# Kernel optimization log

Hardware: AMD Instinct MI355X
Metric: run time of the kernel (lower is better)

The kernel has to match this reference:

```python
import jax, jax.numpy as jnp
import numpy as np

B, S, F_IN, H, NH, NL, HOR = 8, 128, 128, 256, 8, 4, 24


def _ln(x, g, b, eps=1e-5):
    m = jnp.mean(x, axis=-1, keepdims=True)
    v = jnp.var(x, axis=-1, keepdims=True)
    return (x - m) / jnp.sqrt(v + eps) * g + b


def setup_inputs() -> dict:
    key = jax.random.key(0)
    cnt = [0]
    def nrm(shape, scale=0.02):
        cnt[0] += 1
        return jax.random.normal(jax.random.fold_in(key, cnt[0]), shape, jnp.float32) * scale
    d = {}
    d['x'] = jax.random.normal(jax.random.fold_in(key, 999), (B, S, F_IN), jnp.float32)
    # flattened GRN (input F_IN -> hidden H -> output F_IN)
    d['fg_w1'] = nrm((F_IN, H)); d['fg_b1'] = nrm((H,))
    d['fg_w2'] = nrm((H, H));    d['fg_b2'] = nrm((H,))
    d['fg_wo'] = nrm((H, F_IN)); d['fg_bo'] = nrm((F_IN,))
    d['fg_wg'] = nrm((H, F_IN)); d['fg_bg'] = nrm((F_IN,))
    d['fg_sw'] = nrm((F_IN, F_IN)); d['fg_sb'] = nrm((F_IN,))
    d['fg_lng'] = jnp.ones((F_IN,)); d['fg_lnb'] = jnp.zeros((F_IN,))
    # stacked per-variable GRNs (input 1 -> hidden H -> output H), F_IN of them
    d['sv_w1'] = nrm((F_IN, H)); d['sv_b1'] = nrm((F_IN, H))
    d['sv_w2'] = nrm((F_IN, H, H)); d['sv_b2'] = nrm((F_IN, H))
    d['sv_wo'] = nrm((F_IN, H, H)); d['sv_bo'] = nrm((F_IN, H))
    d['sv_wg'] = nrm((F_IN, H, H)); d['sv_bg'] = nrm((F_IN, H))
    d['sv_sw'] = nrm((F_IN, H)); d['sv_sb'] = nrm((F_IN, H))
    d['sv_lng'] = jnp.ones((F_IN, H)); d['sv_lnb'] = jnp.zeros((F_IN, H))
    d['pos_enc'] = nrm((1000, H), 1.0)
    # 2-layer LSTM (torch gate order i,f,g,o)
    for l in (0, 1):
        d[f'l{l}_wih'] = nrm((4 * H, H)); d[f'l{l}_whh'] = nrm((4 * H, H))
        d[f'l{l}_bih'] = nrm((4 * H,));   d[f'l{l}_bhh'] = nrm((4 * H,))
    # NL attention layers, stacked
    d['att_wq'] = nrm((NL, H, H)); d['att_wk'] = nrm((NL, H, H))
    d['att_wv'] = nrm((NL, H, H)); d['att_wo'] = nrm((NL, H, H))
    d['att_bo'] = nrm((NL, H))
    d['att_lng'] = jnp.ones((NL, H)); d['att_lnb'] = jnp.zeros((NL, H))
    # output head and quantile heads
    d['out_w1'] = nrm((H, H // 2)); d['out_b1'] = nrm((H // 2,))
    d['out_w2'] = nrm((H // 2, HOR)); d['out_b2'] = nrm((HOR,))
    d['qw'] = nrm((3, H, HOR)); d['qb'] = nrm((3, HOR))
    return d


def _forward(x, fg_w1, fg_b1, fg_w2, fg_b2, fg_wo, fg_bo, fg_wg, fg_bg, fg_sw, fg_sb,
             fg_lng, fg_lnb, sv_w1, sv_b1, sv_w2, sv_b2, sv_wo, sv_bo, sv_wg, sv_bg,
             sv_sw, sv_sb, sv_lng, sv_lnb, pos_enc, l0_wih, l0_whh, l0_bih, l0_bhh,
             l1_wih, l1_whh, l1_bih, l1_bhh, att_wq, att_wk, att_wv, att_wo, att_bo,
             att_lng, att_lnb, out_w1, out_b1, out_w2, out_b2, qw, qb):
    b, s, f = x.shape
    xf = x.reshape(b * s, f)                      # [N,F]
    # ---- flattened GRN -> variable selection weights ----
    skip = xf @ fg_sw + fg_sb
    h = jax.nn.elu(xf @ fg_w1 + fg_b1)
    h = jax.nn.elu(h @ fg_w2 + fg_b2)
    sw = _ln(jax.nn.sigmoid(h @ fg_wg + fg_bg) * (h @ fg_wo + fg_bo) + skip, fg_lng, fg_lnb)
    sw = jax.nn.softmax(sw, axis=-1)              # [N,F]
    # ---- all per-variable GRNs, batched over the feature axis ----
    h1 = jax.nn.elu(xf[:, :, None] * sv_w1[None] + sv_b1[None])                 # [N,F,H]
    h2 = jax.nn.elu(jnp.einsum('nfh,fhk->nfk', h1, sv_w2) + sv_b2)              # [N,F,H]
    vo = jnp.einsum('nfh,fhk->nfk', h2, sv_wo) + sv_bo
    vg = jax.nn.sigmoid(jnp.einsum('nfh,fhk->nfk', h2, sv_wg) + sv_bg)
    vskip = xf[:, :, None] * sv_sw[None] + sv_sb[None]
    v = _ln(vg * vo + vskip, sv_lng, sv_lnb)                                    # [N,F,H]
    sel = jnp.einsum('nfh,nf->nh', v, sw)                                       # [N,H]
    feats = sel.reshape(b, s, -1) + pos_enc[:s][None]                           # [B,S,H]
    # ---- 2-layer LSTM ----
    def lstm(xseq, wih, whh, bih, bhh):
        hh = whh.shape[1]
        bias = bih + bhh
        def step(carry, xt):
            hp, cp = carry
            g = xt @ wih.T + hp @ whh.T + bias
            i, fg, gg, o = jnp.split(g, 4, axis=-1)
            c = jax.nn.sigmoid(fg) * cp + jax.nn.sigmoid(i) * jnp.tanh(gg)
            hn = jax.nn.sigmoid(o) * jnp.tanh(c)
            return (hn, c), hn
        init = (jnp.zeros((xseq.shape[0], hh), xseq.dtype),
                jnp.zeros((xseq.shape[0], hh), xseq.dtype))
        _, ys = jax.lax.scan(step, init, jnp.swapaxes(xseq, 0, 1))
        return jnp.swapaxes(ys, 0, 1)
    a = lstm(feats, l0_wih, l0_whh, l0_bih, l0_bhh)
    a = lstm(a, l1_wih, l1_whh, l1_bih, l1_bhh)
    # ---- NL self-attention layers ----
    dk = a.shape[-1] // NH
    scale = 1.0 / np.sqrt(dk)
    for l in range(att_wq.shape[0]):
        resid = a
        Q = (a @ att_wq[l]).reshape(b, s, NH, dk)
        K = (a @ att_wk[l]).reshape(b, s, NH, dk)
        V = (a @ att_wv[l]).reshape(b, s, NH, dk)
        scores = jnp.einsum('bqhd,bkhd->bhqk', Q, K) * scale
        w = jax.nn.softmax(scores, axis=-1)
        ctx = jnp.einsum('bhqk,bkhd->bqhd', w, V).reshape(b, s, -1)
        a = _ln(ctx @ att_wo[l] + att_bo[l] + resid, att_lng[l], att_lnb[l])
    gctx = jnp.mean(a, axis=1)                                                  # [B,H]
    pf = jax.nn.relu(gctx @ out_w1 + out_b1) @ out_w2 + out_b2                  # [B,HOR]
    q10 = gctx @ qw[0] + qb[0]
    q50 = gctx @ qw[1] + qb[1]
    q90 = gctx @ qw[2] + qb[2]
    return pf, q10, q50, q90, sw.reshape(b, s, -1), a


def reference(x, fg_w1, fg_b1, fg_w2, fg_b2, fg_wo, fg_bo, fg_wg, fg_bg, fg_sw, fg_sb,
              fg_lng, fg_lnb, sv_w1, sv_b1, sv_w2, sv_b2, sv_wo, sv_bo, sv_wg, sv_bg,
              sv_sw, sv_sb, sv_lng, sv_lnb, pos_enc, l0_wih, l0_whh, l0_bih, l0_bhh,
              l1_wih, l1_whh, l1_bih, l1_bhh, att_wq, att_wk, att_wv, att_wo, att_bo,
              att_lng, att_lnb, out_w1, out_b1, out_w2, out_b2, qw, qb):
    return _forward(x, fg_w1, fg_b1, fg_w2, fg_b2, fg_wo, fg_bo, fg_wg, fg_bg, fg_sw,
                    fg_sb, fg_lng, fg_lnb, sv_w1, sv_b1, sv_w2, sv_b2, sv_wo, sv_bo,
                    sv_wg, sv_bg, sv_sw, sv_sb, sv_lng, sv_lnb, pos_enc, l0_wih, l0_whh,
                    l0_bih, l0_bhh, l1_wih, l1_whh, l1_bih, l1_bhh, att_wq, att_wk,
                    att_wv, att_wo, att_bo, att_lng, att_lnb, out_w1, out_b1, out_w2,
                    out_b2, qw, qb)
```

## Files before the change

### kernel.cpp

```cpp
#include <hip/hip_runtime.h>
#include <cstdint>
#include <cstddef>

typedef __bf16 bf16;
typedef __attribute__((ext_vector_type(4))) __bf16 bf16x4;
typedef __attribute__((ext_vector_type(8))) __bf16 bf16x8;
typedef __attribute__((ext_vector_type(4))) float floatx4;

#define MFMA16(a,b,c) __builtin_amdgcn_mfma_f32_16x16x32_bf16(a,b,c,0,0,0)

__device__ __forceinline__ float sigmf_(float x){ return 1.f/(1.f+expf(-x)); }
__device__ __forceinline__ float eluf_(float x){ return x>0.f ? x : (expf(x)-1.f); }

template<int EPI>
__global__ void __launch_bounds__(256, 2)
gemm_bf16(const float* __restrict__ A, int lda,
          const bf16* __restrict__ BT, int ldb,
          float* __restrict__ C, int ldc,
          const float* __restrict__ b1, const float* __restrict__ b2r,
          int K)
{
  __shared__ char sm[16384 + 8192];
  const int tid = threadIdx.x;
  const int bm = blockIdx.y * 128, bn = blockIdx.x * 64;
  const int l = tid & 63, w = tid >> 6;
  const int wm = (w >> 1) * 64, wn = (w & 1) * 32;
  floatx4 acc[4][2];
  #pragma unroll
  for (int i = 0; i < 4; ++i)
    #pragma unroll
    for (int j = 0; j < 2; ++j)
      #pragma unroll
      for (int r = 0; r < 4; ++r) acc[i][j][r] = 0.f;

  for (int k0 = 0; k0 < K; k0 += 64) {
    {
      int r0 = tid >> 4, kq = (tid & 15) * 4;
      #pragma unroll
      for (int p = 0; p < 8; ++p) {
        int m = r0 + p * 16;
        float4 v = *(const float4*)(A + (size_t)(bm + m) * lda + k0 + kq);
        bf16x4 hv; hv[0]=(bf16)v.x; hv[1]=(bf16)v.y; hv[2]=(bf16)v.z; hv[3]=(bf16)v.w;
        unsigned off = ((unsigned)(m * 128 + kq * 2)) ^ ((unsigned)(m & 7) << 4);
        *(bf16x4*)(sm + off) = hv;
      }
      int n = tid >> 2, c = (tid & 3) * 16;
      const bf16* src = BT + (size_t)(bn + n) * ldb + k0 + c;
      bf16x8 v0 = *(const bf16x8*)(src);
      bf16x8 v1 = *(const bf16x8*)(src + 8);
      unsigned o0 = 16384u + (((unsigned)(n * 128 + c * 2))      ^ ((unsigned)(n & 7) << 4));
      unsigned o1 = 16384u + (((unsigned)(n * 128 + c * 2 + 16)) ^ ((unsigned)(n & 7) << 4));
      *(bf16x8*)(sm + o0) = v0;
      *(bf16x8*)(sm + o1) = v1;
    }
    __syncthreads();
    const int row = l & 15, kb = (l >> 4) * 8;
    #pragma unroll
    for (int kk = 0; kk < 64; kk += 32) {
      bf16x8 a[4], b[2];
      #pragma unroll
      for (int i = 0; i < 4; ++i) {
        int m = wm + i * 16 + row;
        unsigned off = ((unsigned)(m * 128 + (kk + kb) * 2)) ^ ((unsigned)(m & 7) << 4);
        a[i] = *(const bf16x8*)(sm + off);
      }
      #pragma unroll
      for (int j = 0; j < 2; ++j) {
        int n = wn + j * 16 + row;
        unsigned off = 16384u + (((unsigned)(n * 128 + (kk + kb) * 2)) ^ ((unsigned)(n & 7) << 4));
        b[j] = *(const bf16x8*)(sm + off);
      }
      #pragma unroll
      for (int i = 0; i < 4; ++i)
        #pragma unroll
        for (int j = 0; j < 2; ++j)
          acc[i][j] = MFMA16(a[i], b[j], acc[i][j]);
    }
    __syncthreads();
  }
  #pragma unroll
  for (int i = 0; i < 4; ++i)
    #pragma unroll
    for (int j = 0; j < 2; ++j)
      #pragma unroll
      for (int r = 0; r < 4; ++r) {
        int grow = bm + wm + i * 16 + ((l >> 4) << 2) + r;
        int gcol = bn + wn + j * 16 + (l & 15);
        float v = acc[i][j][r];
        if (EPI == 1) v += b1[gcol];
        else if (EPI == 2) { v += b1[gcol]; v = eluf_(v); }
        else if (EPI == 3) { v += (gcol < 128) ? b1[gcol] : b2r[gcol - 128]; }
        else if (EPI == 4) { v += b1[gcol] + b2r[(size_t)grow * ldc + gcol]; }
        C[(size_t)grow * ldc + gcol] = v;
      }
}

__device__ __forceinline__ void tile_tr64(const float* __restrict__ src, int srcld,
                                          bf16* __restrict__ dst, int dstld,
                                          float (*ld)[72])
{
  const int tid = threadIdx.x;
  const int r = tid >> 2, q = tid & 3;
  #pragma unroll
  for (int i = 0; i < 4; ++i) {
    int col = q * 16 + i * 4;
    *(float4*)&ld[r][col] = *(const float4*)(src + (size_t)r * srcld + col);
  }
  __syncthreads();
  bf16x8 o0, o1;
  #pragma unroll
  for (int i = 0; i < 8; ++i) o0[i] = (bf16)ld[q * 16 + i][r];
  #pragma unroll
  for (int i = 0; i < 8; ++i) o1[i] = (bf16)ld[q * 16 + 8 + i][r];
  *(bf16x8*)(dst + (size_t)r * dstld + q * 16) = o0;
  *(bf16x8*)(dst + (size_t)r * dstld + q * 16 + 8) = o1;
}

__global__ void __launch_bounds__(256)
transpose_sv(const float* __restrict__ w2, const float* __restrict__ wo,
             const float* __restrict__ wg, bf16* __restrict__ svT)
{
  __shared__ float ld[64][72];
  int mat = blockIdx.y >> 7;
  int f = blockIdx.y & 127;
  const float* src = (mat == 0 ? w2 : (mat == 1 ? wo : wg)) + (size_t)f * 65536;
  bf16* dst = svT + (size_t)blockIdx.y * 65536;
  int tc = blockIdx.x & 3, tr = blockIdx.x >> 2;
  tile_tr64(src + (size_t)(tr * 64) * 256 + tc * 64, 256,
            dst + (size_t)(tc * 64) * 256 + tr * 64, 256, ld);
}

struct TJob { const float* src; bf16* dst; int R; int C; };
struct TJobs { TJob j[22]; };

__global__ void __launch_bounds__(256)
transpose_misc(TJobs jobs)
{
  __shared__ float ld[64][72];
  TJob J = jobs.j[blockIdx.y];
  int ntc = J.C >> 6;
  int tiles = (J.R >> 6) * ntc;
  if ((int)blockIdx.x >= tiles) return;
  int tc = blockIdx.x % ntc, tr = blockIdx.x / ntc;
  tile_tr64(J.src + (size_t)(tr * 64) * J.C + tc * 64, J.C,
            J.dst + (size_t)(tc * 64) * J.R + tr * 64, J.R, ld);
}

__global__ void __launch_bounds__(256)
cvt4_kernel(const float* __restrict__ s0, const float* __restrict__ s1,
            const float* __restrict__ s2, const float* __restrict__ s3,
            bf16* __restrict__ dst)
{
  size_t i = ((size_t)blockIdx.x * 256 + threadIdx.x) * 4;
  int mat = (int)(i >> 18);
  const float* s = (mat == 0) ? s0 : (mat == 1) ? s1 : (mat == 2) ? s2 : s3;
  float4 v = *(const float4*)(s + (i & 262143));
  bf16x4 o; o[0]=(bf16)v.x; o[1]=(bf16)v.y; o[2]=(bf16)v.z; o[3]=(bf16)v.w;
  *(bf16x4*)(dst + i) = o;
}

__global__ void __launch_bounds__(256, 4)
grnflat_sw_kernel(const float* __restrict__ go, const float* __restrict__ skip,
                  const float* __restrict__ lng, const float* __restrict__ lnb,
                  float* __restrict__ sw_out)
{
  const int tid = threadIdx.x;
  const int m = blockIdx.x * 4 + (tid >> 6);
  const int l = tid & 63, c = l * 2;
  float g0 = go[(size_t)m * 256 + c],       g1 = go[(size_t)m * 256 + c + 1];
  float o0 = go[(size_t)m * 256 + 128 + c], o1 = go[(size_t)m * 256 + 128 + c + 1];
  float sk0 = skip[(size_t)m * 128 + c],    sk1 = skip[(size_t)m * 128 + c + 1];
  float p0 = sigmf_(g0) * o0 + sk0;
  float p1 = sigmf_(g1) * o1 + sk1;
  float s = p0 + p1, s2 = p0 * p0 + p1 * p1;
  #pragma unroll
  for (int k = 1; k < 64; k <<= 1) { s += __shfl_xor(s, k, 64); s2 += __shfl_xor(s2, k, 64); }
  float mean = s * (1.f / 128.f);
  float var = s2 * (1.f / 128.f) - mean * mean;
  float rs = rsqrtf(var + 1e-5f);
  float t0 = (p0 - mean) * rs * lng[c] + lnb[c];
  float t1 = (p1 - mean) * rs * lng[c + 1] + lnb[c + 1];
  float mx = fmaxf(t0, t1);
  #pragma unroll
  for (int k = 1; k < 64; k <<= 1) mx = fmaxf(mx, __shfl_xor(mx, k, 64));
  float e0 = expf(t0 - mx), e1 = expf(t1 - mx);
  float se = e0 + e1;
  #pragma unroll
  for (int k = 1; k < 64; k <<= 1) se += __shfl_xor(se, k, 64);
  float inv = 1.f / se;
  float2 wv; wv.x = e0 * inv; wv.y = e1 * inv;
  *(float2*)(sw_out + (size_t)m * 128 + c) = wv;
}

__global__ void __launch_bounds__(512, 2)
pervar_kernel(const bf16* __restrict__ xT, const bf16* __restrict__ svT,
              const float* __restrict__ w1g, const float* __restrict__ b1g,
              const float* __restrict__ b2g, const float* __restrict__ bog,
              const float* __restrict__ bgg, const float* __restrict__ swg,
              const float* __restrict__ sbg, const float* __restrict__ lngg,
              const float* __restrict__ lnbg,
              bf16* __restrict__ vbuf, int f0)
{
  __shared__ char sm[65536];
  const int tid = threadIdx.x;
  const int fl = blockIdx.y, f = f0 + fl, tile = blockIdx.x;
  const int l = tid & 63, w = tid >> 6;
  const int wm = (w >> 2) * 32, wn = (w & 3) * 64;
  const int row = l & 15, kb = (l >> 4) * 8;
  const size_t fb = (size_t)f * 256;

  {
    int m = tid >> 3, ks8 = (tid & 7) * 32;
    float x = (float)xT[(size_t)f * 1024 + tile * 64 + m];
    #pragma unroll
    for (int i = 0; i < 4; ++i) {
      int k = ks8 + i * 8;
      float4 w0v = *(const float4*)(w1g + fb + k);
      float4 w1v = *(const float4*)(w1g + fb + k + 4);
      float4 b0v = *(const float4*)(b1g + fb + k);
      float4 b1v = *(const float4*)(b1g + fb + k + 4);
      bf16x8 hv;
      hv[0] = (bf16)eluf_(x * w0v.x + b0v.x);
      hv[1] = (bf16)eluf_(x * w0v.y + b0v.y);
      hv[2] = (bf16)eluf_(x * w0v.z + b0v.z);
      hv[3] = (bf16)eluf_(x * w0v.w + b0v.w);
      hv[4] = (bf16)eluf_(x * w1v.x + b1v.x);
      hv[5] = (bf16)eluf_(x * w1v.y + b1v.y);
      hv[6] = (bf16)eluf_(x * w1v.z + b1v.z);
      hv[7] = (bf16)eluf_(x * w1v.w + b1v.w);
      unsigned off = ((unsigned)(m * 512 + k * 2)) ^ ((unsigned)(m & 7) << 4);
      *(bf16x8*)(sm + off) = hv;
    }
  }

  auto stageB = [&](const bf16* BT, int ks) {
    int n = tid >> 1, c = (tid & 1) * 32;
    const bf16* src = BT + (size_t)n * 256 + ks * 64 + c;
    #pragma unroll
    for (int qq = 0; qq < 4; ++qq) {
      unsigned ro = (((unsigned)(n * 128 + (c + qq * 8) * 2)) ^ ((unsigned)(n & 7) << 4));
      *(bf16x8*)(sm + 32768 + ro) = *(const bf16x8*)(src + qq * 8);
    }
  };

  floatx4 acc1[2][4];
  #pragma unroll
  for (int i = 0; i < 2; ++i)
    #pragma unroll
    for (int j = 0; j < 4; ++j)
      #pragma unroll
      for (int r = 0; r < 4; ++r) acc1[i][j][r] = 0.f;
  const bf16* w2T = svT + (size_t)f * 65536;
  for (int ks = 0; ks < 4; ++ks) {
    __syncthreads();
    stageB(w2T, ks);
    __syncthreads();
    #pragma unroll
    for (int kk = 0; kk < 64; kk += 32) {
      int kloc = kk + kb;
      bf16x8 a[2], b[4];
      #pragma unroll
      for (int i = 0; i < 2; ++i) {
        int m = wm + i * 16 + row;
        unsigned off = ((unsigned)(m * 512 + (ks * 64 + kloc) * 2)) ^ ((unsigned)(m & 7) << 4);
        a[i] = *(const bf16x8*)(sm + off);
      }
      #pragma unroll
      for (int j = 0; j < 4; ++j) {
        int n = wn + j * 16 + row;
        unsigned off = 32768u + (((unsigned)(n * 128 + kloc * 2)) ^ ((unsigned)(n & 7) << 4));
        b[j] = *(const bf16x8*)(sm + off);
      }
      #pragma unroll
      for (int i = 0; i < 2; ++i)
        #pragma unroll
        for (int j = 0; j < 4; ++j)
          acc1[i][j] = MFMA16(a[i], b[j], acc1[i][j]);
    }
  }
  __syncthreads();
  #pragma unroll
  for (int i = 0; i < 2; ++i)
    #pragma unroll
    for (int j = 0; j < 4; ++j)
      #pragma unroll
      for (int r = 0; r < 4; ++r) {
        int m = wm + i * 16 + ((l >> 4) << 2) + r;
        int col = wn + j * 16 + (l & 15);
        float v = eluf_(acc1[i][j][r] + b2g[fb + col]);
        unsigned off = ((unsigned)(m * 512 + col * 2)) ^ ((unsigned)(m & 7) << 4);
        *(bf16*)(sm + off) = (bf16)v;
      }
  __syncthreads();

  floatx4 accO[2][4], accG[2][4];
  #pragma unroll
  for (int i = 0; i < 2; ++i)
    #pragma unroll
    for (int j = 0; j < 4; ++j)
      #pragma unroll
      for (int r = 0; r < 4; ++r) { accO[i][j][r] = 0.f; accG[i][j][r] = 0.f; }
  const bf16* woT = svT + ((size_t)128 + f) * 65536;
  const bf16* wgT = svT + ((size_t)256 + f) * 65536;
  for (int ks = 0; ks < 4; ++ks) {
    __syncthreads();
    stageB(woT, ks);
    __syncthreads();
    #pragma unroll
    for (int kk = 0; kk < 64; kk += 32) {
      int kloc = kk + kb;
      bf16x8 a[2], b[4];
      #pragma unroll
      for (int i = 0; i < 2; ++i) {
        int m = wm + i * 16 + row;
        unsigned off = ((unsigned)(m * 512 + (ks * 64 + kloc) * 2)) ^ ((unsigned)(m & 7) << 4);
        a[i] = *(const bf16x8*)(sm + off);
      }
      #pragma unroll
      for (int j = 0; j < 4; ++j) {
        int n = wn + j * 16 + row;
        unsigned off = 32768u + (((unsigned)(n * 128 + kloc * 2)) ^ ((unsigned)(n & 7) << 4));
        b[j] = *(const bf16x8*)(sm + off);
      }
      #pragma unroll
      for (int i = 0; i < 2; ++i)
        #pragma unroll
        for (int j = 0; j < 4; ++j)
          accO[i][j] = MFMA16(a[i], b[j], accO[i][j]);
    }
  }
  for (int ks = 0; ks < 4; ++ks) {
    __syncthreads();
    stageB(wgT, ks);
    __syncthreads();
    #pragma unroll
    for (int kk = 0; kk < 64; kk += 32) {
      int kloc = kk + kb;
      bf16x8 a[2], b[4];
      #pragma unroll
      for (int i = 0; i < 2; ++i) {
        int m = wm + i * 16 + row;
        unsigned off = ((unsigned)(m * 512 + (ks * 64 + kloc) * 2)) ^ ((unsigned)(m & 7) << 4);
        a[i] = *(const bf16x8*)(sm + off);
      }
      #pragma unroll
      for (int j = 0; j < 4; ++j) {
        int n = wn + j * 16 + row;
        unsigned off = 32768u + (((unsigned)(n * 128 + kloc * 2)) ^ ((unsigned)(n & 7) << 4));
        b[j] = *(const bf16x8*)(sm + off);
      }
      #pragma unroll
      for (int i = 0; i < 2; ++i)
        #pragma unroll
        for (int j = 0; j < 4; ++j)
          accG[i][j] = MFMA16(a[i], b[j], accG[i][j]);
    }
  }
  __syncthreads();
  {
    float xm[2][4];
    #pragma unroll
    for (int i = 0; i < 2; ++i)
      #pragma unroll
      for (int r = 0; r < 4; ++r) {
        int m = wm + i * 16 + ((l >> 4) << 2) + r;
        xm[i][r] = (float)xT[(size_t)f * 1024 + tile * 64 + m];
      }
    #pragma unroll
    for (int i = 0; i < 2; ++i)
      #pragma unroll
      for (int j = 0; j < 4; ++j)
        #pragma unroll
        for (int r = 0; r < 4; ++r) {
          int m = wm + i * 16 + ((l >> 4) << 2) + r;
          int col = wn + j * 16 + (l & 15);
          float vg = sigmf_(accG[i][j][r] + bgg[fb + col]);
          float vo = accO[i][j][r] + bog[fb + col];
          float pre = vg * vo + xm[i][r] * swg[fb + col] + sbg[fb + col];
          unsigned off = ((unsigned)(m * 512 + col * 2)) ^ ((unsigned)(m & 7) << 4);
          *(bf16*)(sm + off) = (bf16)pre;
        }
  }
  __syncthreads();
  {
    int m = tid >> 3, q = tid & 7;
    float vals[32];
    float s = 0.f, s2 = 0.f;
    #pragma unroll
    for (int i = 0; i < 4; ++i) {
      unsigned off = ((unsigned)(m * 512 + (q * 32 + i * 8) * 2)) ^ ((unsigned)(m & 7) << 4);
      bf16x8 hv = *(const bf16x8*)(sm + off);
      #pragma unroll
      for (int j = 0; j < 8; ++j) {
        float x = (float)hv[j];
        vals[i * 8 + j] = x; s += x; s2 += x * x;
      }
    }
    s += __shfl_xor(s, 1, 64);  s += __shfl_xor(s, 2, 64);  s += __shfl_xor(s, 4, 64);
    s2 += __shfl_xor(s2, 1, 64); s2 += __shfl_xor(s2, 2, 64); s2 += __shfl_xor(s2, 4, 64);
    float mean = s * (1.f / 256.f);
    float var = s2 * (1.f / 256.f) - mean * mean;
    float rs = rsqrtf(var + 1e-5f);
    bf16* dst = vbuf + ((size_t)fl * 1024 + tile * 64 + m) * 256 + q * 32;
    #pragma unroll
    for (int i = 0; i < 4; ++i) {
      int c = q * 32 + i * 8;
      float4 g0 = *(const float4*)(lngg + fb + c);
      float4 g1 = *(const float4*)(lngg + fb + c + 4);
      float4 bb0 = *(const float4*)(lnbg + fb + c);
      float4 bb1 = *(const float4*)(lnbg + fb + c + 4);
      bf16x8 ov;
      ov[0] = (bf16)((vals[i * 8 + 0] - mean) * rs * g0.x + bb0.x);
      ov[1] = (bf16)((vals[i * 8 + 1] - mean) * rs * g0.y + bb0.y);
      ov[2] = (bf16)((vals[i * 8 + 2] - mean) * rs * g0.z + bb0.z);
      ov[3] = (bf16)((vals[i * 8 + 3] - mean) * rs * g0.w + bb0.w);
      ov[4] = (bf16)((vals[i * 8 + 4] - mean) * rs * g1.x + bb1.x);
      ov[5] = (bf16)((vals[i * 8 + 5] - mean) * rs * g1.y + bb1.y);
      ov[6] = (bf16)((vals[i * 8 + 6] - mean) * rs * g1.z + bb1.z);
      ov[7] = (bf16)((vals[i * 8 + 7] - mean) * rs * g1.w + bb1.w);
      *(bf16x8*)(dst + i * 8) = ov;
    }
  }
}

__global__ void __launch_bounds__(256, 4)
selreduce_kernel(const bf16* __restrict__ vbuf, const float* __restrict__ sw,
                 const float* __restrict__ pos, float* __restrict__ feats,
                 int f0, int FC, int flags)
{
  const int tid = threadIdx.x;
  const int m = blockIdx.x * 4 + (tid >> 6);
  const int hh = (tid & 63) * 4;
  float a0, a1, a2, a3;
  if (flags & 1) { a0 = a1 = a2 = a3 = 0.f; }
  else {
    float4 v = *(const float4*)(feats + (size_t)m * 256 + hh);
    a0 = v.x; a1 = v.y; a2 = v.z; a3 = v.w;
  }
  for (int fi = 0; fi < FC; ++fi) {
    float wgt = sw[(size_t)m * 128 + f0 + fi];
    bf16x4 v = *(const bf16x4*)(vbuf + ((size_t)fi * 1024 + m) * 256 + hh);
    a0 += wgt * (float)v[0]; a1 += wgt * (float)v[1];
    a2 += wgt * (float)v[2]; a3 += wgt * (float)v[3];
  }
  if (flags & 2) {
    float4 p = *(const float4*)(pos + (size_t)(m & 127) * 256 + hh);
    a0 += p.x; a1 += p.y; a2 += p.z; a3 += p.w;
  }
  float4 o; o.x = a0; o.y = a1; o.z = a2; o.w = a3;
  *(float4*)(feats + (size_t)m * 256 + hh) = o;
}

__global__ void __launch_bounds__(256, 1)
lstm_mfma(const bf16* __restrict__ wl, const float* __restrict__ xpre0,
          const float* __restrict__ b0a, const float* __restrict__ b0b,
          const float* __restrict__ b1a, const float* __restrict__ b1b,
          bf16* __restrict__ h0seq, bf16* __restrict__ h1seq,
          float* __restrict__ aseq, unsigned* __restrict__ ctr)
{
  __shared__ float gbuf[4][16][8];
  const int tid = threadIdx.x;
  const int l = tid & 63, w = tid >> 6;
  const int layer = blockIdx.x >> 4, U = (blockIdx.x & 15) * 16;
  const int row = w * 256 + U + (l & 15);
  const int ko = (l >> 4) * 8;
  const bf16* whh = wl + (size_t)(layer ? 3 : 1) * 262144 + (size_t)row * 256;
  const bf16* wih1 = wl + (size_t)2 * 262144 + (size_t)row * 256;
  bf16x8 bw[8], bx[8];
  #pragma unroll
  for (int kt = 0; kt < 8; ++kt) bw[kt] = *(const bf16x8*)(whh + kt * 32 + ko);
  if (layer) {
    #pragma unroll
    for (int kt = 0; kt < 8; ++kt) bx[kt] = *(const bf16x8*)(wih1 + kt * 32 + ko);
  }
  const float bsum = layer ? (b1a[row] + b1b[row]) : (b0a[row] + b0b[row]);
  bf16* hs = layer ? h1seq : h0seq;
  unsigned* c0 = ctr;
  unsigned* c1 = ctr + 128;
  unsigned* cs = layer ? c1 : c0;
  float cstate = 0.f;
  const int au = tid >> 3, ab = tid & 7;

  for (int t = 0; t < 128; ++t) {
    float xp[4] = {0.f, 0.f, 0.f, 0.f};
    if (!layer && (l >> 4) < 2) {
      #pragma unroll
      for (int r = 0; r < 4; ++r) {
        int bb = (l >> 4) * 4 + r;
        xp[r] = xpre0[((size_t)((bb << 7) | t)) * 1024 + row];
      }
    }
    if (tid == 0) {
      if (layer == 0) {
        if (t > 0)
          while (__hip_atomic_load(c0 + t - 1, __ATOMIC_ACQUIRE, __HIP_MEMORY_SCOPE_AGENT) < 16u)
            __builtin_amdgcn_s_sleep(2);
      } else {
        while (__hip_atomic_load(c0 + t, __ATOMIC_ACQUIRE, __HIP_MEMORY_SCOPE_AGENT) < 16u)
          __builtin_amdgcn_s_sleep(2);
        if (t > 0)
          while (__hip_atomic_load(c1 + t - 1, __ATOMIC_ACQUIRE, __HIP_MEMORY_SCOPE_AGENT) < 16u)
            __builtin_amdgcn_s_sleep(2);
      }
    }
    __syncthreads();
    floatx4 acc; acc[0] = acc[1] = acc[2] = acc[3] = 0.f;
    if (t > 0) {
      const bf16* hp = hs + (size_t)(t - 1) * 4096 + (size_t)(l & 15) * 256 + ko;
      #pragma unroll
      for (int kt = 0; kt < 8; ++kt)
        acc = MFMA16(*(const bf16x8*)(hp + kt * 32), bw[kt], acc);
    }
    if (layer) {
      const bf16* hp = h0seq + (size_t)t * 4096 + (size_t)(l & 15) * 256 + ko;
      #pragma unroll
      for (int kt = 0; kt < 8; ++kt)
        acc = MFMA16(*(const bf16x8*)(hp + kt * 32), bx[kt], acc);
    }
    if ((l >> 4) < 2) {
      #pragma unroll
      for (int r = 0; r < 4; ++r) {
        int bb = (l >> 4) * 4 + r;
        gbuf[w][l & 15][bb] = acc[r] + bsum + xp[r];
      }
    }
    __syncthreads();
    if (tid < 128) {
      float gi = gbuf[0][au][ab], gf = gbuf[1][au][ab];
      float gg = gbuf[2][au][ab], go = gbuf[3][au][ab];
      cstate = sigmf_(gf) * cstate + sigmf_(gi) * tanhf(gg);
      float h = sigmf_(go) * tanhf(cstate);
      hs[(size_t)t * 4096 + (size_t)ab * 256 + U + au] = (bf16)h;
      if (layer) aseq[((size_t)((ab << 7) | t)) * 256 + U + au] = h;
    }
    __syncthreads();
    if (tid == 0) {
      __threadfence();
      __hip_atomic_fetch_add(cs + t, 1u, __ATOMIC_RELEASE, __HIP_MEMORY_SCOPE_AGENT);
    }
  }
}

__global__ void __launch_bounds__(256, 2)
attn_kernel(const float* __restrict__ qkv, float* __restrict__ ctxo)
{
  __shared__ float Kb[128][40];
  __shared__ float Vb[128][40];
  const int tid = threadIdx.x;
  const int b = blockIdx.x >> 3, h = blockIdx.x & 7;
  const int s = tid >> 1, half = tid & 1;
  {
    const float* kr = qkv + ((size_t)(b * 128 + s)) * 768 + 256 + h * 32 + half * 16;
    #pragma unroll
    for (int i = 0; i < 4; ++i) {
      *(float4*)&Kb[s][half * 16 + i * 4] = *(const float4*)(kr + i * 4);
      *(float4*)&Vb[s][half * 16 + i * 4] = *(const float4*)(kr + 256 + i * 4);
    }
  }
  float q[32];
  {
    const float* qr = qkv + ((size_t)(b * 128 + s)) * 768 + h * 32;
    #pragma unroll
    for (int i = 0; i < 8; ++i) {
      float4 v = *(const float4*)(qr + i * 4);
      q[i * 4 + 0] = v.x; q[i * 4 + 1] = v.y; q[i * 4 + 2] = v.z; q[i * 4 + 3] = v.w;
    }
  }
  __syncthreads();
  const float scale = 0.17677669529663687f;
  float se = 0.f;
  float ca[32];
  #pragma unroll
  for (int i = 0; i < 32; ++i) ca[i] = 0.f;
  for (int c0 = 0; c0 < 64; ++c0) {
    int c = half * 64 + c0;
    float d = 0.f;
    #pragma unroll
    for (int i = 0; i < 32; ++i) d += q[i] * Kb[c][i];
    float e = expf(d * scale);
    se += e;
    #pragma unroll
    for (int i = 0; i < 32; ++i) ca[i] += e * Vb[c][i];
  }
  se += __shfl_xor(se, 1, 64);
  #pragma unroll
  for (int i = 0; i < 32; ++i) ca[i] += __shfl_xor(ca[i], 1, 64);
  if (half == 0) {
    float inv = 1.f / se;
    float* outp = ctxo + ((size_t)(b * 128 + s)) * 256 + h * 32;
    #pragma unroll
    for (int i = 0; i < 32; i += 4) {
      float4 v; v.x = ca[i] * inv; v.y = ca[i + 1] * inv; v.z = ca[i + 2] * inv; v.w = ca[i + 3] * inv;
      *(float4*)(outp + i) = v;
    }
  }
}

__global__ void __launch_bounds__(256, 4)
ln_kernel(const float* __restrict__ in, const float* __restrict__ g,
          const float* __restrict__ bta, float* __restrict__ out,
          float* __restrict__ mirror)
{
  const int tid = threadIdx.x;
  const int m = blockIdx.x * 4 + (tid >> 6);
  const int l = tid & 63;
  float4 v = *(const float4*)(in + (size_t)m * 256 + l * 4);
  float s = v.x + v.y + v.z + v.w;
  float s2 = v.x * v.x + v.y * v.y + v.z * v.z + v.w * v.w;
  #pragma unroll
  for (int k = 1; k < 64; k <<= 1) { s += __shfl_xor(s, k, 64); s2 += __shfl_xor(s2, k, 64); }
  float mean = s * (1.f / 256.f);
  float var = s2 * (1.f / 256.f) - mean * mean;
  float rs = rsqrtf(var + 1e-5f);
  float4 gg = *(const float4*)(g + l * 4);
  float4 bb = *(const float4*)(bta + l * 4);
  float4 o;
  o.x = (v.x - mean) * rs * gg.x + bb.x;
  o.y = (v.y - mean) * rs * gg.y + bb.y;
  o.z = (v.z - mean) * rs * gg.z + bb.z;
  o.w = (v.w - mean) * rs * gg.w + bb.w;
  *(float4*)(out + (size_t)m * 256 + l * 4) = o;
  if (mirror) *(float4*)(mirror + (size_t)m * 256 + l * 4) = o;
}

__global__ void __launch_bounds__(256)
gctx_kernel(const float* __restrict__ a, float* __restrict__ g)
{
  int b = blockIdx.x, hh = threadIdx.x;
  float s = 0.f;
  for (int ss = 0; ss < 128; ++ss) s += a[((size_t)b * 128 + ss) * 256 + hh];
  g[b * 256 + hh] = s * (1.f / 128.f);
}

__global__ void __launch_bounds__(256, 1)
head_kernel(const float* __restrict__ g, const float* __restrict__ w1,
            const float* __restrict__ b1, const float* __restrict__ w2,
            const float* __restrict__ b2, const float* __restrict__ qw,
            const float* __restrict__ qb, float* __restrict__ dout)
{
  __shared__ float hid[8][128];
  const int tid = threadIdx.x;
  for (int o = tid; o < 1024; o += 256) {
    int b = o >> 7, j = o & 127;
    float s = b1[j];
    for (int k = 0; k < 256; ++k) s += g[b * 256 + k] * w1[(size_t)k * 128 + j];
    hid[b][j] = s > 0.f ? s : 0.f;
  }
  __syncthreads();
  if (tid < 192) {
    int b = tid / 24, j = tid - b * 24;
    float s = b2[j];
    for (int k = 0; k < 128; ++k) s += hid[b][k] * w2[(size_t)k * 24 + j];
    dout[b * 24 + j] = s;
  }
  for (int o = tid; o < 576; o += 256) {
    int qi = o / 192, rr = o - qi * 192, b = rr / 24, j = rr - b * 24;
    float s = qb[qi * 24 + j];
    for (int k = 0; k < 256; ++k) s += g[b * 256 + k] * qw[((size_t)qi * 256 + k) * 24 + j];
    dout[192 + o] = s;
  }
}

extern "C" void kernel_launch(void* const* d_in, const int* in_sizes, int n_in,
                              void* d_out, int out_size, void* d_ws, size_t ws_size,
                              hipStream_t stream)
{
  (void)in_sizes; (void)n_in; (void)out_size;
  auto F = [&](int i) { return (const float*)d_in[i]; };
  char* ws = (char*)d_ws;
  size_t o = 0;
  auto alloc = [&](size_t b) { size_t r = o; o = (o + b + 255) & ~(size_t)255; return r; };

  size_t svT_o  = alloc((size_t)3 * 128 * 65536 * 2);
  size_t wl_o   = alloc((size_t)4 * 262144 * 2);
  size_t qkvT_o = alloc((size_t)4 * 196608 * 2);
  size_t woT_o  = alloc((size_t)4 * 65536 * 2);
  size_t w1T_o  = alloc(256 * 128 * 2);
  size_t w2T_o  = alloc(256 * 256 * 2);
  size_t goT_o  = alloc(256 * 256 * 2);
  size_t swT_o  = alloc(128 * 128 * 2);
  size_t xT_o   = alloc(128 * 1024 * 2);
  size_t h_o    = alloc((size_t)1024 * 256 * 4);
  size_t h2_o   = alloc((size_t)1024 * 256 * 4);
  size_t go_o   = alloc((size_t)1024 * 256 * 4);
  size_t skip_o = alloc((size_t)1024 * 128 * 4);
  size_t feat_o = alloc((size_t)1024 * 256 * 4);
  size_t xpre_o = alloc((size_t)1024 * 1024 * 4);
  size_t qkv_o  = alloc((size_t)1024 * 768 * 4);
  size_t ctx_o  = alloc((size_t)1024 * 256 * 4);
  size_t pre_o  = alloc((size_t)1024 * 256 * 4);
  size_t aA_o   = alloc((size_t)1024 * 256 * 4);
  size_t aB_o   = alloc((size_t)1024 * 256 * 4);
  size_t gctx_o = alloc(8 * 256 * 4);
  size_t z_o    = alloc((size_t)2 * 1048576 + 1024);
  size_t aseq_o = alloc((size_t)1024 * 256 * 4);
  int FC = 128;
  while (FC > 4 && o + (size_t)FC * 1024 * 256 * 2 > ws_size) FC >>= 1;
  size_t vb_o = alloc((size_t)FC * 1024 * 256 * 2);
  if (o > ws_size) return;

  bf16* svTp  = (bf16*)(ws + svT_o);
  bf16* wlp   = (bf16*)(ws + wl_o);
  bf16* qkvTp = (bf16*)(ws + qkvT_o);
  bf16* woTp  = (bf16*)(ws + woT_o);
  bf16* w1Tp  = (bf16*)(ws + w1T_o);
  bf16* w2Tp  = (bf16*)(ws + w2T_o);
  bf16* goTp  = (bf16*)(ws + goT_o);
  bf16* swTp  = (bf16*)(ws + swT_o);
  bf16* xTp   = (bf16*)(ws + xT_o);
  float* hp    = (float*)(ws + h_o);
  float* h2p   = (float*)(ws + h2_o);
  float* gop   = (float*)(ws + go_o);
  float* skipp = (float*)(ws + skip_o);
  float* featp = (float*)(ws + feat_o);
  float* xprep = (float*)(ws + xpre_o);
  float* qkvp  = (float*)(ws + qkv_o);
  float* ctxp  = (float*)(ws + ctx_o);
  float* prep  = (float*)(ws + pre_o);
  float* aAp   = (float*)(ws + aA_o);
  float* aBp   = (float*)(ws + aB_o);
  float* gctxp = (float*)(ws + gctx_o);
  bf16* h0p    = (bf16*)(ws + z_o);
  bf16* h1p    = (bf16*)(ws + z_o + 1048576);
  unsigned* ctrp = (unsigned*)(ws + z_o + 2097152);
  float* aseqp = (float*)(ws + aseq_o);
  bf16* vbp    = (bf16*)(ws + vb_o);

  float* outp  = (float*)d_out;
  float* sw_do = outp + 768;
  float* a_do  = outp + 131840;

  hipMemsetAsync(ws + z_o, 0, 2097152 + 1024, stream);

  transpose_sv<<<dim3(16, 384), 256, 0, stream>>>(F(15), F(17), F(19), svTp);
  {
    TJobs tj; int nj = 0;
    auto addj = [&](const float* s, bf16* d, int R, int C) { tj.j[nj].src = s; tj.j[nj].dst = d; tj.j[nj].R = R; tj.j[nj].C = C; ++nj; };
    for (int l = 0; l < 4; ++l) {
      addj(F(34) + (size_t)l * 65536, qkvTp + (size_t)l * 196608, 256, 256);
      addj(F(35) + (size_t)l * 65536, qkvTp + (size_t)l * 196608 + 65536, 256, 256);
      addj(F(36) + (size_t)l * 65536, qkvTp + (size_t)l * 196608 + 131072, 256, 256);
      addj(F(37) + (size_t)l * 65536, woTp + (size_t)l * 65536, 256, 256);
    }
    addj(F(1), w1Tp, 128, 256);
    addj(F(3), w2Tp, 256, 256);
    addj(F(7), goTp, 256, 128);
    addj(F(5), goTp + 128 * 256, 256, 128);
    addj(F(9), swTp, 128, 128);
    addj(F(0), xTp, 1024, 128);
    transpose_misc<<<dim3(32, 22), 256, 0, stream>>>(tj);
  }
  cvt4_kernel<<<1024, 256, 0, stream>>>(F(26), F(27), F(30), F(31), wlp);

  auto gemm = [&](int epi, const float* A, int lda, const bf16* BT, int ldb,
                  float* C, int ldc, int M, int N, int K,
                  const float* b1, const float* b2r) {
    dim3 g(N / 64, M / 128);
    switch (epi) {
      case 0: gemm_bf16<0><<<g, 256, 0, stream>>>(A, lda, BT, ldb, C, ldc, b1, b2r, K); break;
      case 1: gemm_bf16<1><<<g, 256, 0, stream>>>(A, lda, BT, ldb, C, ldc, b1, b2r, K); break;
      case 2: gemm_bf16<2><<<g, 256, 0, stream>>>(A, lda, BT, ldb, C, ldc, b1, b2r, K); break;
      case 3: gemm_bf16<3><<<g, 256, 0, stream>>>(A, lda, BT, ldb, C, ldc, b1, b2r, K); break;
      case 4: gemm_bf16<4><<<g, 256, 0, stream>>>(A, lda, BT, ldb, C, ldc, b1, b2r, K); break;
    }
  };

  gemm(2, F(0), 128, w1Tp, 128, hp, 256, 1024, 256, 128, F(2), nullptr);
  gemm(2, hp, 256, w2Tp, 256, h2p, 256, 1024, 256, 256, F(4), nullptr);
  gemm(3, h2p, 256, goTp, 256, gop, 256, 1024, 256, 256, F(8), F(6));
  gemm(1, F(0), 128, swTp, 128, skipp, 128, 1024, 128, 128, F(10), nullptr);
  grnflat_sw_kernel<<<256, 256, 0, stream>>>(gop, skipp, F(11), F(12), sw_do);

  int chunks = 128 / FC;
  for (int c = 0; c < chunks; ++c) {
    pervar_kernel<<<dim3(16, FC), 512, 0, stream>>>(
        xTp, svTp, F(13), F(14), F(16), F(18), F(20), F(21), F(22), F(23), F(24),
        vbp, c * FC);
    selreduce_kernel<<<256, 256, 0, stream>>>(
        vbp, sw_do, F(25), featp, c * FC, FC,
        (c == 0 ? 1 : 0) | (c == chunks - 1 ? 2 : 0));
  }

  gemm(0, featp, 256, wlp, 256, xprep, 1024, 1024, 1024, 256, nullptr, nullptr);
  lstm_mfma<<<32, 256, 0, stream>>>(wlp, xprep, F(28), F(29), F(32), F(33),
                                    h0p, h1p, aseqp, ctrp);

  const float* ain = aseqp;
  float* louts[4] = {aAp, aBp, aAp, aBp};
  for (int l = 0; l < 4; ++l) {
    gemm(0, ain, 256, qkvTp + (size_t)l * 196608, 256, qkvp, 768, 1024, 768, 256, nullptr, nullptr);
    attn_kernel<<<64, 256, 0, stream>>>(qkvp, ctxp);
    gemm(4, ctxp, 256, woTp + (size_t)l * 65536, 256, prep, 256, 1024, 256, 256,
         F(38) + (size_t)l * 256, ain);
    ln_kernel<<<256, 256, 0, stream>>>(prep, F(39) + (size_t)l * 256, F(40) + (size_t)l * 256,
                                       louts[l], l == 3 ? a_do : (float*)nullptr);
    ain = louts[l];
  }

  gctx_kernel<<<8, 256, 0, stream>>>(aBp, gctxp);
  head_kernel<<<1, 256, 0, stream>>>(gctxp, F(41), F(42), F(43), F(44), F(45), F(46), outp);
}
```

Before: 1.112 ms.

## Fuse QKV projection into attention and output projection with LayerNorm

Each attention block now computes its own Q/K/V slice with MFMA, reading the layer input directly, so the separate QKV GEMM and its global buffer are gone. The output projection, bias, residual add and LayerNorm are merged into one kernel where each block owns 128 full rows. This cuts four launches down to two per layer and removes intermediate global round trips. The trade-off is that every (batch, head) block re-reads its full input rows and QKV weights are loaded from global without LDS staging. The proj_ln kernel runs on only 8 blocks, which leaves most of the GPU idle.

```diff
diff --git a/kernel.cpp b/kernel.cpp
--- a/kernel.cpp
+++ b/kernel.cpp
@@ -541,32 +541,77 @@
   }
 }
 
-__global__ void __launch_bounds__(256, 2)
-attn_kernel(const float* __restrict__ qkv, float* __restrict__ ctxo)
-{
-  __shared__ float Kb[128][40];
-  __shared__ float Vb[128][40];
+__global__ void __launch_bounds__(256, 1)
+attn_qkv(const float* __restrict__ a, const bf16* __restrict__ qkvT,
+         float* __restrict__ ctxo)
+{
+  extern __shared__ char sm[];
+  float* Qb = (float*)(sm + 65536);
+  float* Kb = (float*)(sm + 86016);
+  float* Vb = (float*)(sm + 106496);
   const int tid = threadIdx.x;
   const int b = blockIdx.x >> 3, h = blockIdx.x & 7;
+  const int l = tid & 63, w = tid >> 6;
+  {
+    int m = tid >> 1, ch = (tid & 1) * 128;
+    const float* src = a + (size_t)(b * 128 + m) * 256 + ch;
+    #pragma unroll
+    for (int cc = 0; cc < 16; ++cc) {
+      float4 v0 = *(const float4*)(src + cc * 8);
+      float4 v1 = *(const float4*)(src + cc * 8 + 4);
+      bf16x8 hv;
+      hv[0]=(bf16)v0.x; hv[1]=(bf16)v0.y; hv[2]=(bf16)v0.z; hv[3]=(bf16)v0.w;
+      hv[4]=(bf16)v1.x; hv[5]=(bf16)v1.y; hv[6]=(bf16)v1.z; hv[7]=(bf16)v1.w;
+      int k = ch + cc * 8;
+      unsigned off = ((unsigned)(m * 512 + k * 2)) ^ ((unsigned)(m & 7) << 4);
+      *(bf16x8*)(sm + off) = hv;
+    }
+  }
+  __syncthreads();
+  const int row = l & 15, kb = (l >> 4) * 8;
+  floatx4 acc[2][6];
+  #pragma unroll
+  for (int i = 0; i < 2; ++i)
+    #pragma unroll
+    for (int j = 0; j < 6; ++j)
+      #pragma unroll
+      for (int r = 0; r < 4; ++r) acc[i][j][r] = 0.f;
+  for (int k0 = 0; k0 < 256; k0 += 32) {
+    int kloc = k0 + kb;
+    bf16x8 af[2];
+    #pragma unroll
+    for (int i = 0; i < 2; ++i) {
+      int m = 32 * w + 16 * i + row;
+      unsigned off = ((unsigned)(m * 512 + kloc * 2)) ^ ((unsigned)(m & 7) << 4);
+      af[i] = *(const bf16x8*)(sm + off);
+    }
+    #pragma unroll
+    for (int j = 0; j < 6; ++j) {
+      int nn = h * 32 + (j & 1) * 16 + row;
+      const bf16* bp = qkvT + (size_t)(j >> 1) * 65536 + (size_t)nn * 256 + kloc;
+      bf16x8 bf_ = *(const bf16x8*)bp;
+      #pragma unroll
+      for (int i = 0; i < 2; ++i)
+        acc[i][j] = MFMA16(af[i], bf_, acc[i][j]);
+    }
+  }
+  #pragma unroll
+  for (int i = 0; i < 2; ++i)
+    #pragma unroll
+    for (int j = 0; j < 6; ++j) {
+      float* dst = (j >> 1) == 0 ? Qb : ((j >> 1) == 1 ? Kb : Vb);
+      #pragma unroll
+      for (int r = 0; r < 4; ++r) {
+        int m = 32 * w + 16 * i + ((l >> 4) << 2) + r;
+        int nn = (j & 1) * 16 + (l & 15);
+        dst[m * 40 + nn] = acc[i][j][r];
+      }
+    }
+  __syncthreads();
   const int s = tid >> 1, half = tid & 1;
-  {
-    const float* kr = qkv + ((size_t)(b * 128 + s)) * 768 + 256 + h * 32 + half * 16;
-    #pragma unroll
-    for (int i = 0; i < 4; ++i) {
-      *(float4*)&Kb[s][half * 16 + i * 4] = *(const float4*)(kr + i * 4);
-      *(float4*)&Vb[s][half * 16 + i * 4] = *(const float4*)(kr + 256 + i * 4);
-    }
-  }
   float q[32];
-  {
-    const float* qr = qkv + ((size_t)(b * 128 + s)) * 768 + h * 32;
-    #pragma unroll
-    for (int i = 0; i < 8; ++i) {
-      float4 v = *(const float4*)(qr + i * 4);
-      q[i * 4 + 0] = v.x; q[i * 4 + 1] = v.y; q[i * 4 + 2] = v.z; q[i * 4 + 3] = v.w;
-    }
-  }
-  __syncthreads();
+  #pragma unroll
+  for (int i = 0; i < 32; ++i) q[i] = Qb[s * 40 + i];
   const float scale = 0.17677669529663687f;
   float se = 0.f;
   float ca[32];
@@ -576,11 +621,11 @@
     int c = half * 64 + c0;
     float d = 0.f;
     #pragma unroll
-    for (int i = 0; i < 32; ++i) d += q[i] * Kb[c][i];
+    for (int i = 0; i < 32; ++i) d += q[i] * Kb[c * 40 + i];
     float e = expf(d * scale);
     se += e;
     #pragma unroll
-    for (int i = 0; i < 32; ++i) ca[i] += e * Vb[c][i];
+    for (int i = 0; i < 32; ++i) ca[i] += e * Vb[c * 40 + i];
   }
   se += __shfl_xor(se, 1, 64);
   #pragma unroll
@@ -596,31 +641,95 @@
   }
 }
 
-__global__ void __launch_bounds__(256, 4)
-ln_kernel(const float* __restrict__ in, const float* __restrict__ g,
-          const float* __restrict__ bta, float* __restrict__ out,
-          float* __restrict__ mirror)
-{
+__global__ void __launch_bounds__(256, 1)
+proj_ln(const float* __restrict__ A, const bf16* __restrict__ BT,
+        const float* __restrict__ bias, const float* __restrict__ resid,
+        const float* __restrict__ g, const float* __restrict__ bta,
+        float* __restrict__ out, float* __restrict__ mirror)
+{
+  __shared__ char sm[16384 + 32768];
   const int tid = threadIdx.x;
-  const int m = blockIdx.x * 4 + (tid >> 6);
-  const int l = tid & 63;
-  float4 v = *(const float4*)(in + (size_t)m * 256 + l * 4);
-  float s = v.x + v.y + v.z + v.w;
-  float s2 = v.x * v.x + v.y * v.y + v.z * v.z + v.w * v.w;
-  #pragma unroll
-  for (int k = 1; k < 64; k <<= 1) { s += __shfl_xor(s, k, 64); s2 += __shfl_xor(s2, k, 64); }
-  float mean = s * (1.f / 256.f);
-  float var = s2 * (1.f / 256.f) - mean * mean;
-  float rs = rsqrtf(var + 1e-5f);
-  float4 gg = *(const float4*)(g + l * 4);
-  float4 bb = *(const float4*)(bta + l * 4);
-  float4 o;
-  o.x = (v.x - mean) * rs * gg.x + bb.x;
-  o.y = (v.y - mean) * rs * gg.y + bb.y;
-  o.z = (v.z - mean) * rs * gg.z + bb.z;
-  o.w = (v.w - mean) * rs * gg.w + bb.w;
-  *(float4*)(out + (size_t)m * 256 + l * 4) = o;
-  if (mirror) *(float4*)(mirror + (size_t)m * 256 + l * 4) = o;
+  const int bm = blockIdx.x * 128;
+  const int l = tid & 63, w = tid >> 6;
+  const int row = l & 15, kb = (l >> 4) * 8;
+  floatx4 acc[2][16];
+  #pragma unroll
+  for (int i = 0; i < 2; ++i)
+    #pragma unroll
+    for (int j = 0; j < 16; ++j)
+      #pragma unroll
+      for (int r = 0; r < 4; ++r) acc[i][j][r] = 0.f;
+
+  for (int k0 = 0; k0 < 256; k0 += 64) {
+    {
+      int r0 = tid >> 4, kq = (tid & 15) * 4;
+      #pragma unroll
+      for (int p = 0; p < 8; ++p) {
+        int m = r0 + p * 16;
+        float4 v = *(const float4*)(A + (size_t)(bm + m) * 256 + k0 + kq);
+        bf16x4 hv; hv[0]=(bf16)v.x; hv[1]=(bf16)v.y; hv[2]=(bf16)v.z; hv[3]=(bf16)v.w;
+        unsigned off = ((unsigned)(m * 128 + kq * 2)) ^ ((unsigned)(m & 7) << 4);
+        *(bf16x4*)(sm + off) = hv;
+      }
+      int n = tid;
+      const bf16* src = BT + (size_t)n * 256 + k0;
+      #pragma unroll
+      for (int qq = 0; qq < 8; ++qq) {
+        unsigned ro = 16384u + (((unsigned)(n * 128 + qq * 16)) ^ ((unsigned)(n & 7) << 4));
+        *(bf16x8*)(sm + ro) = *(const bf16x8*)(src + qq * 8);
+      }
+    }
+    __syncthreads();
+    #pragma unroll
+    for (int kk = 0; kk < 64; kk += 32) {
+      int kloc = kk + kb;
+      bf16x8 af[2];
+      #pragma unroll
+      for (int i = 0; i < 2; ++i) {
+        int m = 32 * w + 16 * i + row;
+        unsigned off = ((unsigned)(m * 128 + kloc * 2)) ^ ((unsigned)(m & 7) << 4);
+        af[i] = *(const bf16x8*)(sm + off);
+      }
+      #pragma unroll
+      for (int j = 0; j < 16; ++j) {
+        int n = 16 * j + row;
+        unsigned off = 16384u + (((unsigned)(n * 128 + kloc * 2)) ^ ((unsigned)(n & 7) << 4));
+        bf16x8 bf_ = *(const bf16x8*)(sm + off);
+        #pragma unroll
+        for (int i = 0; i < 2; ++i)
+          acc[i][j] = MFMA16(af[i], bf_, acc[i][j]);
+      }
+    }
+    __syncthreads();
+  }
+  #pragma unroll
+  for (int i = 0; i < 2; ++i)
+    #pragma unroll
+    for (int r = 0; r < 4; ++r) {
+      int grow = bm + 32 * w + 16 * i + ((l >> 4) << 2) + r;
+      float vv[16];
+      float s = 0.f, s2 = 0.f;
+      #pragma unroll
+      for (int j = 0; j < 16; ++j) {
+        int gcol = 16 * j + (l & 15);
+        float v = acc[i][j][r] + bias[gcol] + resid[(size_t)grow * 256 + gcol];
+        vv[j] = v; s += v; s2 += v * v;
+      }
+      s += __shfl_xor(s, 1, 64);  s += __shfl_xor(s, 2, 64);
+      s += __shfl_xor(s, 4, 64);  s += __shfl_xor(s, 8, 64);
+      s2 += __shfl_xor(s2, 1, 64); s2 += __shfl_xor(s2, 2, 64);
+      s2 += __shfl_xor(s2, 4, 64); s2 += __shfl_xor(s2, 8, 64);
+      float mean = s * (1.f / 256.f);
+      float var = s2 * (1.f / 256.f) - mean * mean;
+      float rs = rsqrtf(var + 1e-5f);
+      #pragma unroll
+      for (int j = 0; j < 16; ++j) {
+        int gcol = 16 * j + (l & 15);
+        float o = (vv[j] - mean) * rs * g[gcol] + bta[gcol];
+        out[(size_t)grow * 256 + gcol] = o;
+        if (mirror) mirror[(size_t)grow * 256 + gcol] = o;
+      }
+    }
 }
 
 __global__ void __launch_bounds__(256)
@@ -686,9 +795,7 @@
   size_t skip_o = alloc((size_t)1024 * 128 * 4);
   size_t feat_o = alloc((size_t)1024 * 256 * 4);
   size_t xpre_o = alloc((size_t)1024 * 1024 * 4);
-  size_t qkv_o  = alloc((size_t)1024 * 768 * 4);
   size_t ctx_o  = alloc((size_t)1024 * 256 * 4);
-  size_t pre_o  = alloc((size_t)1024 * 256 * 4);
   size_t aA_o   = alloc((size_t)1024 * 256 * 4);
   size_t aB_o   = alloc((size_t)1024 * 256 * 4);
   size_t gctx_o = alloc(8 * 256 * 4);
@@ -714,9 +821,7 @@
   float* skipp = (float*)(ws + skip_o);
   float* featp = (float*)(ws + feat_o);
   float* xprep = (float*)(ws + xpre_o);
-  float* qkvp  = (float*)(ws + qkv_o);
   float* ctxp  = (float*)(ws + ctx_o);
-  float* prep  = (float*)(ws + pre_o);
   float* aAp   = (float*)(ws + aA_o);
   float* aBp   = (float*)(ws + aB_o);
   float* gctxp = (float*)(ws + gctx_o);
@@ -731,6 +836,8 @@
   float* a_do  = outp + 131840;
 
   hipMemsetAsync(ws + z_o, 0, 2097152 + 1024, stream);
+  hipFuncSetAttribute((const void*)attn_qkv,
+                      hipFuncAttributeMaxDynamicSharedMemorySize, 126976);
 
   transpose_sv<<<dim3(16, 384), 256, 0, stream>>>(F(15), F(17), F(19), svTp);
   {
@@ -788,12 +895,11 @@
   const float* ain = aseqp;
   float* louts[4] = {aAp, aBp, aAp, aBp};
   for (int l = 0; l < 4; ++l) {
-    gemm(0, ain, 256, qkvTp + (size_t)l * 196608, 256, qkvp, 768, 1024, 768, 256, nullptr, nullptr);
-    attn_kernel<<<64, 256, 0, stream>>>(qkvp, ctxp);
-    gemm(4, ctxp, 256, woTp + (size_t)l * 65536, 256, prep, 256, 1024, 256, 256,
-         F(38) + (size_t)l * 256, ain);
-    ln_kernel<<<256, 256, 0, stream>>>(prep, F(39) + (size_t)l * 256, F(40) + (size_t)l * 256,
-                                       louts[l], l == 3 ? a_do : (float*)nullptr);
+    attn_qkv<<<64, 256, 126976, stream>>>(ain, qkvTp + (size_t)l * 196608, ctxp);
+    proj_ln<<<8, 256, 0, stream>>>(ctxp, woTp + (size_t)l * 65536,
+                                   F(38) + (size_t)l * 256, ain,
+                                   F(39) + (size_t)l * 256, F(40) + (size_t)l * 256,
+                                   louts[l], l == 3 ? a_do : (float*)nullptr);
     ain = louts[l];
   }
 
```

New measurement: 1.299 ms. 16.8% more time.
